# Optimization experiments

Hardware: AMD Instinct MI355X
Metric: run time of the kernel (lower is better)

The kernel has to match this reference:

```python
import jax, jax.numpy as jnp
import numpy as np

N, E = 50000, 800000
IN_DIM, OUT_DIM, H = 256, 128, 8
GEO_HID = 16  # RBF feature dim and geo_mlp hidden dim


def setup_inputs() -> dict:
    key = jax.random.key(0)
    ks = jax.random.split(key, 16)
    def lin(k, fan_out, fan_in):
        kw, kb = jax.random.split(k)
        lim = 1.0 / np.sqrt(fan_in)
        W = jax.random.uniform(kw, (fan_out, fan_in), jnp.float32, -lim, lim)
        b = jax.random.uniform(kb, (fan_out,), jnp.float32, -lim, lim)
        return W, b
    Wq, bq = lin(ks[0], OUT_DIM, IN_DIM)
    Wk, bk = lin(ks[1], OUT_DIM, IN_DIM)
    Wv, bv = lin(ks[2], OUT_DIM, IN_DIM)
    Wo, bo = lin(ks[3], OUT_DIM, OUT_DIM)
    Wg1, bg1 = lin(ks[4], GEO_HID, GEO_HID)
    Wg2, bg2 = lin(ks[5], H, GEO_HID)
    x = jax.random.normal(ks[6], (N, IN_DIM), jnp.float32)
    edge_index = jax.random.randint(ks[7], (2, E), 0, N, jnp.int64)
    edge_dist = jax.random.uniform(ks[8], (E,), jnp.float32) * 6.0
    return {"x": x, "edge_index": edge_index, "edge_dist": edge_dist,
            "Wq": Wq, "bq": bq, "Wk": Wk, "bk": bk, "Wv": Wv, "bv": bv,
            "Wo": Wo, "bo": bo, "Wg1": Wg1, "bg1": bg1, "Wg2": Wg2, "bg2": bg2}


def reference(x, edge_index, edge_dist, Wq, bq, Wk, bk, Wv, bv, Wo, bo, Wg1, bg1, Wg2, bg2):
    n = x.shape[0]
    num_heads = Wg2.shape[0]
    head_dim = Wq.shape[0] // num_heads
    scale = 1.0 / (head_dim ** 0.5)

    q = (x @ Wq.T + bq).reshape(n, num_heads, head_dim)
    k = (x @ Wk.T + bk).reshape(n, num_heads, head_dim)
    v = (x @ Wv.T + bv).reshape(n, num_heads, head_dim)

    # RBF expansion: 16 centers in [0, 6], gamma = 1.0
    centers = jnp.linspace(0.0, 6.0, GEO_HID)
    rbf = jnp.exp(-(edge_dist[:, None] - centers) ** 2)          # [E, 16]
    geo_bias = jax.nn.relu(rbf @ Wg1.T + bg1) @ Wg2.T + bg2      # [E, H]

    row, col = edge_index[0], edge_index[1]
    attn = (q[row] * k[col]).sum(-1) * scale + geo_bias          # [E, H]

    # segment softmax over incoming edges per destination node (row)
    m = jax.ops.segment_max(attn, row, num_segments=n)           # [N, H]
    e = jnp.exp(attn - m[row])
    s = jax.ops.segment_sum(e, row, num_segments=n)              # [N, H]
    a = e / (s[row] + 1e-12)                                     # [E, H]

    out = jax.ops.segment_sum(v[col] * a[:, :, None], row, num_segments=n)
    out = out.reshape(n, num_heads * head_dim)
    return out @ Wo.T + bo
```

## Files before the change

kernel.cpp:

```cpp
#include <hip/hip_runtime.h>
#include <math.h>

#define IN_DIM 256
#define OUT_DIM 128
#define NH 8
#define HD 16
#define GH 16
#define TBL 1024
#define LOG2E 1.44269504f
#define RCAP 64
#define BINSH 6
#define BCAP 1408

typedef __attribute__((ext_vector_type(8))) short short8;
typedef __attribute__((ext_vector_type(4))) float floatx4;

__device__ __forceinline__ unsigned short f2bf(float f) {
    union { float f; unsigned u; } v; v.f = f;
    unsigned r = v.u + 0x7fffu + ((v.u >> 16) & 1u);
    return (unsigned short)(r >> 16);
}
__device__ __forceinline__ float bf2f(unsigned short h) {
    union { unsigned u; float f; } v; v.u = ((unsigned)h) << 16;
    return v.f;
}
__device__ __forceinline__ void split1(float f, unsigned short& h, unsigned short& l) {
    h = f2bf(f);
    l = f2bf(f - bf2f(h));
}
__device__ __forceinline__ float bflo(unsigned u) { return __uint_as_float(u << 16); }
__device__ __forceinline__ float bfhi(unsigned u) { return __uint_as_float(u & 0xffff0000u); }

__global__ __launch_bounds__(256) void prep_all_kernel(
    const float* __restrict__ Wq, const float* __restrict__ Wk,
    const float* __restrict__ Wv, const float* __restrict__ Wo,
    unsigned short* __restrict__ wh, unsigned short* __restrict__ wl,
    unsigned short* __restrict__ wo_h, unsigned short* __restrict__ wo_l,
    const float* __restrict__ Wg1, const float* __restrict__ bg1,
    const float* __restrict__ Wg2, const float* __restrict__ bg2,
    float* __restrict__ tbl, int* __restrict__ gbin,
    int nbins, int nwm, int nwo, int ngeo) {
    int bx = blockIdx.x;
    int t = threadIdx.x;

    if (bx < 3 * nwm) {
        int m = bx / nwm;
        int i = (bx - m * nwm) * 256 + t;
        if (i >= (OUT_DIM * IN_DIM) / 4) return;
        const float* W = (m == 0) ? Wq : (m == 1) ? Wk : Wv;
        float4 f = ((const float4*)W)[i];
        ushort4 h, l;
        split1(f.x, h.x, l.x); split1(f.y, h.y, l.y);
        split1(f.z, h.z, l.z); split1(f.w, h.w, l.w);
        size_t base = (size_t)m * (OUT_DIM * IN_DIM) / 4;
        ((ushort4*)wh)[base + i] = h;
        ((ushort4*)wl)[base + i] = l;
        return;
    }
    bx -= 3 * nwm;
    if (bx < nwo) {
        int i = bx * 256 + t;
        if (i >= (OUT_DIM * OUT_DIM) / 4) return;
        float4 f = ((const float4*)Wo)[i];
        ushort4 h, l;
        split1(f.x, h.x, l.x); split1(f.y, h.y, l.y);
        split1(f.z, h.z, l.z); split1(f.w, h.w, l.w);
        ((ushort4*)wo_h)[i] = h;
        ((ushort4*)wo_l)[i] = l;
        return;
    }
    bx -= nwo;
    if (bx < ngeo) {
        int i = bx * 256 + t;
        if (i >= TBL) return;
        float d = (float)i * (6.0f / (float)(TBL - 1));
        float rbf[GH];
#pragma unroll
        for (int j = 0; j < GH; ++j) {
            float c = 0.4f * (float)j;
            float tt = d - c;
            rbf[j] = __expf(-tt * tt);
        }
        float hid[GH];
#pragma unroll
        for (int j = 0; j < GH; ++j) {
            float acc = bg1[j];
#pragma unroll
            for (int kk = 0; kk < GH; ++kk) acc += rbf[kk] * Wg1[j * GH + kk];
            hid[j] = fmaxf(acc, 0.0f);
        }
#pragma unroll
        for (int h = 0; h < NH; ++h) {
            float acc = bg2[h];
#pragma unroll
            for (int j = 0; j < GH; ++j) acc += hid[j] * Wg2[h * GH + j];
            tbl[i * NH + h] = acc * LOG2E;
        }
        return;
    }
    for (int i = t; i < nbins; i += 256) gbin[i] = 0;
}

__global__ __launch_bounds__(512, 4) void qkv_kernel(
    const float* __restrict__ x,
    const unsigned short* __restrict__ wh, const unsigned short* __restrict__ wl,
    const float* __restrict__ bq, const float* __restrict__ bk, const float* __restrict__ bv,
    float* __restrict__ q, unsigned short* __restrict__ kb, unsigned short* __restrict__ vb,
    const int* __restrict__ ei, const float* __restrict__ edist,
    int* __restrict__ gbin, int2* __restrict__ binbuf,
    int Nn, int E_, int nxb, int nb1, int nbins) {
    __shared__ unsigned short xh_s[128 * 40];
    __shared__ unsigned short xl_s[128 * 40];
    __shared__ unsigned short wh_s[128 * 40];
    __shared__ unsigned short wl_s[128 * 40];

    const int tid = threadIdx.x;
    int bx = blockIdx.x;

    if (bx < nb1) {
        int* hist_s = (int*)xh_s;
        const int e0 = bx * 4096;
        for (int b = tid; b < nbins; b += 512) hist_s[b] = 0;
        __syncthreads();
#pragma unroll
        for (int i = 0; i < 8; ++i) {
            int e = e0 + tid + i * 512;
            if (e < E_) atomicAdd(&hist_s[ei[e] >> BINSH], 1);
        }
        __syncthreads();
        for (int b = tid; b < nbins; b += 512) {
            int h = hist_s[b];
            int base = 0;
            if (h) base = atomicAdd(&gbin[b], h);
            hist_s[b] = base;
        }
        __syncthreads();
#pragma unroll
        for (int i = 0; i < 8; ++i) {
            int e = e0 + tid + i * 512;
            if (e < E_) {
                int row = ei[e];
                int bin = row >> BINSH;
                int r = atomicAdd(&hist_s[bin], 1);
                float u = edist[e] * ((float)(TBL - 1) / 6.0f);
                u = fminf(fmaxf(u, 0.0f), (float)(TBL - 1));
                if (r < BCAP)
                    binbuf[(size_t)bin * BCAP + r] =
                        make_int2((ei[E_ + e] & 0x1FFFF) | ((row & 63) << 17), __float_as_int(u));
            }
        }
        return;
    }
    bx -= nb1;

    const int wsel = bx / nxb;
    const int n0 = (bx - wsel * nxb) * 128;
    const unsigned short* W_h = wh + (size_t)wsel * (OUT_DIM * IN_DIM);
    const unsigned short* W_l = wl + (size_t)wsel * (OUT_DIM * IN_DIM);
    const float* bias = (wsel == 0) ? bq : (wsel == 1) ? bk : bv;
    const bool vpath = (wsel == 2);

    const int w = tid >> 6;
    const int lane = tid & 63;
    const int ml = lane & 15;
    const int quad = lane >> 4;
    const int rg = w & 3;
    const int cg = w >> 2;

    const int rows_valid = min(128, Nn - n0);

    floatx4 acc[2][4];
#pragma unroll
    for (int rr = 0; rr < 2; ++rr)
#pragma unroll
        for (int ct = 0; ct < 4; ++ct) acc[rr][ct] = (floatx4){0.f, 0.f, 0.f, 0.f};

    const int r = tid >> 2, c = tid & 3;
    const bool rvld = (r < rows_valid);
    const float* xrow = x + (size_t)(n0 + r) * IN_DIM + c * 8;
    const unsigned short* wrow_h = W_h + (size_t)r * IN_DIM + c * 8;
    const unsigned short* wrow_l = W_l + (size_t)r * IN_DIM + c * 8;

    float4 xa = {0.f, 0.f, 0.f, 0.f}, xb = {0.f, 0.f, 0.f, 0.f};
    short8 wreg_h, wreg_l;
    if (rvld) { xa = ((const float4*)xrow)[0]; xb = ((const float4*)xrow)[1]; }
    wreg_h = *(const short8*)(wrow_h);
    if (vpath) wreg_l = *(const short8*)(wrow_l);

    for (int kci = 0; kci < 8; ++kci) {
        {
            float xf[8] = {xa.x, xa.y, xa.z, xa.w, xb.x, xb.y, xb.z, xb.w};
            if (!vpath) {
                unsigned short hv[8];
#pragma unroll
                for (int j = 0; j < 8; ++j) hv[j] = f2bf(xf[j]);
                *(short8*)(xh_s + r * 40 + c * 8) = *(short8*)hv;
                *(short8*)(wh_s + r * 40 + c * 8) = wreg_h;
            } else {
                unsigned short hv[8], lv[8];
#pragma unroll
                for (int j = 0; j < 8; ++j) split1(xf[j], hv[j], lv[j]);
                *(short8*)(xh_s + r * 40 + c * 8) = *(short8*)hv;
                *(short8*)(xl_s + r * 40 + c * 8) = *(short8*)lv;
                *(short8*)(wh_s + r * 40 + c * 8) = wreg_h;
                *(short8*)(wl_s + r * 40 + c * 8) = wreg_l;
            }
        }
        __syncthreads();

        if (kci < 7) {
            const int koff = (kci + 1) * 32;
            if (rvld) {
                xa = ((const float4*)(xrow + koff))[0];
                xb = ((const float4*)(xrow + koff))[1];
            }
            wreg_h = *(const short8*)(wrow_h + koff);
            if (vpath) wreg_l = *(const short8*)(wrow_l + koff);
        }

        short8 ah0 = *(const short8*)(xh_s + (rg * 32 + ml) * 40 + quad * 8);
        short8 ah1 = *(const short8*)(xh_s + (rg * 32 + 16 + ml) * 40 + quad * 8);
        if (!vpath) {
#pragma unroll
            for (int ct = 0; ct < 4; ++ct) {
                short8 bh = *(const short8*)(wh_s + (cg * 64 + ct * 16 + ml) * 40 + quad * 8);
                acc[0][ct] = __builtin_amdgcn_mfma_f32_16x16x32_bf16(ah0, bh, acc[0][ct], 0, 0, 0);
                acc[1][ct] = __builtin_amdgcn_mfma_f32_16x16x32_bf16(ah1, bh, acc[1][ct], 0, 0, 0);
            }
        } else {
            short8 al0 = *(const short8*)(xl_s + (rg * 32 + ml) * 40 + quad * 8);
            short8 al1 = *(const short8*)(xl_s + (rg * 32 + 16 + ml) * 40 + quad * 8);
#pragma unroll
            for (int ct = 0; ct < 4; ++ct) {
                short8 bh = *(const short8*)(wh_s + (cg * 64 + ct * 16 + ml) * 40 + quad * 8);
                short8 bl = *(const short8*)(wl_s + (cg * 64 + ct * 16 + ml) * 40 + quad * 8);
                acc[0][ct] = __builtin_amdgcn_mfma_f32_16x16x32_bf16(ah0, bh, acc[0][ct], 0, 0, 0);
                acc[0][ct] = __builtin_amdgcn_mfma_f32_16x16x32_bf16(al0, bh, acc[0][ct], 0, 0, 0);
                acc[0][ct] = __builtin_amdgcn_mfma_f32_16x16x32_bf16(ah0, bl, acc[0][ct], 0, 0, 0);
                acc[1][ct] = __builtin_amdgcn_mfma_f32_16x16x32_bf16(ah1, bh, acc[1][ct], 0, 0, 0);
                acc[1][ct] = __builtin_amdgcn_mfma_f32_16x16x32_bf16(al1, bh, acc[1][ct], 0, 0, 0);
                acc[1][ct] = __builtin_amdgcn_mfma_f32_16x16x32_bf16(ah1, bl, acc[1][ct], 0, 0, 0);
            }
        }
        __syncthreads();
    }

    if (wsel == 0) {
#pragma unroll
        for (int rr = 0; rr < 2; ++rr)
#pragma unroll
            for (int ct = 0; ct < 4; ++ct) {
                int col = cg * 64 + ct * 16 + ml;
                float bj = bias[col];
#pragma unroll
                for (int rr2 = 0; rr2 < 4; ++rr2) {
                    int grow = n0 + rg * 32 + rr * 16 + quad * 4 + rr2;
                    if (grow < Nn) q[(size_t)grow * 128 + col] = acc[rr][ct][rr2] + bj;
                }
            }
    } else {
        unsigned short* ob = (wsel == 1) ? kb : vb;
#pragma unroll
        for (int rr = 0; rr < 2; ++rr)
#pragma unroll
            for (int ct = 0; ct < 4; ++ct) {
                int col = cg * 64 + ct * 16 + ml;
                float bj = bias[col];
#pragma unroll
                for (int rr2 = 0; rr2 < 4; ++rr2) {
                    int grow = n0 + rg * 32 + rr * 16 + quad * 4 + rr2;
                    if (grow < Nn) ob[(size_t)grow * 128 + col] = f2bf(acc[rr][ct][rr2] + bj);
                }
            }
    }
}

__global__ __launch_bounds__(256) void bin2bucket_kernel(
    const int2* __restrict__ binbuf, const int* __restrict__ gbin,
    int2* __restrict__ bucket, int2* __restrict__ meta, int Nn) {
    __shared__ int rcnt[64];
    __shared__ int pref[64];
    __shared__ int2 ebuf[BCAP];
    const int bin = blockIdx.x;
    const int t = threadIdx.x;
    if (t < 64) rcnt[t] = 0;
    __syncthreads();
    int nb = gbin[bin];
    if (nb > BCAP) nb = BCAP;
    const int row0 = bin << BINSH;

    int px[6], py[6], rk[6];
#pragma unroll
    for (int j = 0; j < 6; ++j) {
        int i = t + j * 256;
        rk[j] = -1;
        if (i < nb) {
            int2 p = binbuf[(size_t)bin * BCAP + i];
            int rowrel = (p.x >> 17) & 63;
            int r = atomicAdd(&rcnt[rowrel], 1);
            if (r < RCAP) { px[j] = p.x & 0x1FFFF; py[j] = p.y; rk[j] = r | (rowrel << 16); }
        }
    }
    __syncthreads();
    int myclamp = 0;
    if (t < 64) { myclamp = min(rcnt[t], RCAP); pref[t] = myclamp; }
    __syncthreads();
    for (int off = 1; off < 64; off <<= 1) {
        int v = 0;
        if (t < 64 && t >= off) v = pref[t - off];
        __syncthreads();
        if (t < 64) pref[t] += v;
        __syncthreads();
    }
#pragma unroll
    for (int j = 0; j < 6; ++j) {
        if (rk[j] >= 0) {
            int rowrel = rk[j] >> 16;
            int r = rk[j] & 0xFFFF;
            int pos = pref[rowrel] - min(rcnt[rowrel], RCAP) + r;
            ebuf[pos] = make_int2(px[j], py[j]);
        }
    }
    __syncthreads();
    int total = pref[63];
    const int obase = bin * BCAP;
    for (int i = t; i < total; i += 256) bucket[obase + i] = ebuf[i];
    if (t < 64 && row0 + t < Nn)
        meta[row0 + t] = make_int2(obase + pref[t] - myclamp, myclamp);
}

__global__ __launch_bounds__(256) void fused_node_kernel(
    const float* __restrict__ q, const unsigned short* __restrict__ kb,
    const unsigned short* __restrict__ vb, const int2* __restrict__ bucket,
    const float* __restrict__ tbl, const int2* __restrict__ meta,
    float* __restrict__ o, int Nn) {
    const int lane = threadIdx.x & 63;
    const int g = lane >> 3;
    const int h = lane & 7;
    const int n = blockIdx.x * 4 + (threadIdx.x >> 6);
    if (n >= Nn) return;

    const int2 m = meta[n];
    const int start = m.x;
    const int c = m.y;
    const int end = start + c;

    float qf[16];
    {
        const float4* qp = (const float4*)(q + (size_t)n * 128 + h * 16);
#pragma unroll
        for (int j = 0; j < 4; ++j) {
            float4 t = qp[j];
            qf[j * 4 + 0] = t.x; qf[j * 4 + 1] = t.y;
            qf[j * 4 + 2] = t.z; qf[j * 4 + 3] = t.w;
        }
    }

    float l = 0.0f;
    float acc[16];
#pragma unroll
    for (int j = 0; j < 16; ++j) acc[j] = 0.0f;

    auto edge_math = [&](const uint4& k0, const uint4& k1, const uint4& v0, const uint4& v1,
                         float u, bool valid) {
        unsigned kk[8] = {k0.x, k0.y, k0.z, k0.w, k1.x, k1.y, k1.z, k1.w};
        float d = 0.0f;
#pragma unroll
        for (int j = 0; j < 8; ++j) {
            d = fmaf(bflo(kk[j]), qf[2 * j], d);
            d = fmaf(bfhi(kk[j]), qf[2 * j + 1], d);
        }
        int i0 = min((int)u, TBL - 2);
        float fr = u - (float)i0;
        float t0 = tbl[i0 * NH + h];
        float t1 = tbl[i0 * NH + NH + h];
        float logit2 = fmaf(d, 0.25f * LOG2E, fmaf(fr, t1 - t0, t0));
        logit2 = fminf(logit2, 80.0f);
        if (!valid) logit2 = -1e30f;
        float p = __builtin_amdgcn_exp2f(logit2);
        l += p;
        unsigned vv[8] = {v0.x, v0.y, v0.z, v0.w, v1.x, v1.y, v1.z, v1.w};
#pragma unroll
        for (int j = 0; j < 8; ++j) {
            acc[2 * j]     = fmaf(p, bflo(vv[j]), acc[2 * j]);
            acc[2 * j + 1] = fmaf(p, bfhi(vv[j]), acc[2 * j + 1]);
        }
    };

    if (c > 0) {
        int2 npA = bucket[min(start + g, end - 1)];
        const bool vAv = (start + g < end);
        const bool doB = (end > start + 8);
        int2 npB = npA;
        bool vBv = false;
        if (doB) {
            npB = bucket[min(start + 8 + g, end - 1)];
            vBv = (start + 8 + g < end);
        }
        const uint4* kpA = (const uint4*)(kb + (size_t)npA.x * 128 + h * 16);
        const uint4* vpA = (const uint4*)(vb + (size_t)npA.x * 128 + h * 16);
        uint4 kA0 = kpA[0], kA1 = kpA[1], vA0 = vpA[0], vA1 = vpA[1];
        uint4 kB0, kB1, vB0, vB1;
        if (doB) {
            const uint4* kpB = (const uint4*)(kb + (size_t)npB.x * 128 + h * 16);
            const uint4* vpB = (const uint4*)(vb + (size_t)npB.x * 128 + h * 16);
            kB0 = kpB[0]; kB1 = kpB[1]; vB0 = vpB[0]; vB1 = vpB[1];
        }
        edge_math(kA0, kA1, vA0, vA1, __int_as_float(npA.y), vAv);
        if (doB) edge_math(kB0, kB1, vB0, vB1, __int_as_float(npB.y), vBv);
        for (int base = start + 16; base < end; base += 8) {
            int2 np = bucket[min(base + g, end - 1)];
            bool valid = (base + g < end);
            const uint4* kp = (const uint4*)(kb + (size_t)np.x * 128 + h * 16);
            const uint4* vp = (const uint4*)(vb + (size_t)np.x * 128 + h * 16);
            uint4 k0 = kp[0], k1 = kp[1], v0 = vp[0], v1 = vp[1];
            edge_math(k0, k1, v0, v1, __int_as_float(np.y), valid);
        }
    }

#pragma unroll
    for (int off = 8; off < 64; off <<= 1) {
        l += __shfl_xor(l, off);
#pragma unroll
        for (int j = 0; j < 16; ++j) acc[j] += __shfl_xor(acc[j], off);
    }

    if (g == 0) {
        float inv = 1.0f / (l + 1e-12f);
        float4* op = (float4*)(o + (size_t)n * 128 + h * 16);
#pragma unroll
        for (int j = 0; j < 4; ++j) {
            float4 t;
            t.x = acc[j * 4 + 0] * inv; t.y = acc[j * 4 + 1] * inv;
            t.z = acc[j * 4 + 2] * inv; t.w = acc[j * 4 + 3] * inv;
            op[j] = t;
        }
    }
}

__global__ __launch_bounds__(512, 4) void out_gemm_mfma_kernel(
    const float* __restrict__ o,
    const unsigned short* __restrict__ wo_h, const unsigned short* __restrict__ wo_l,
    const float* __restrict__ bo, float* __restrict__ out, int Nn) {
    const int n0 = blockIdx.x * 128;

    __shared__ unsigned short xh_s[128 * 40];
    __shared__ unsigned short xl_s[128 * 40];
    __shared__ unsigned short wh_s[128 * 40];
    __shared__ unsigned short wl_s[128 * 40];

    const int tid = threadIdx.x;
    const int w = tid >> 6;
    const int lane = tid & 63;
    const int ml = lane & 15;
    const int quad = lane >> 4;
    const int rg = w & 3;
    const int cg = w >> 2;

    const int rows_valid = min(128, Nn - n0);

    floatx4 acc[2][4];
#pragma unroll
    for (int rr = 0; rr < 2; ++rr)
#pragma unroll
        for (int ct = 0; ct < 4; ++ct) acc[rr][ct] = (floatx4){0.f, 0.f, 0.f, 0.f};

    const int r = tid >> 2, c = tid & 3;
    const bool rvld = (r < rows_valid);
    const float* orow = o + (size_t)(n0 + r) * OUT_DIM + c * 8;
    const unsigned short* wrow_h = wo_h + (size_t)r * OUT_DIM + c * 8;
    const unsigned short* wrow_l = wo_l + (size_t)r * OUT_DIM + c * 8;

    float4 oa = {0.f, 0.f, 0.f, 0.f}, ob2 = {0.f, 0.f, 0.f, 0.f};
    short8 wreg_h, wreg_l;
    if (rvld) { oa = ((const float4*)orow)[0]; ob2 = ((const float4*)orow)[1]; }
    wreg_h = *(const short8*)(wrow_h);
    wreg_l = *(const short8*)(wrow_l);

    for (int kci = 0; kci < 4; ++kci) {
        {
            float xf[8] = {oa.x, oa.y, oa.z, oa.w, ob2.x, ob2.y, ob2.z, ob2.w};
            unsigned short hv[8], lv[8];
#pragma unroll
            for (int j = 0; j < 8; ++j) split1(xf[j], hv[j], lv[j]);
            *(short8*)(xh_s + r * 40 + c * 8) = *(short8*)hv;
            *(short8*)(xl_s + r * 40 + c * 8) = *(short8*)lv;
            *(short8*)(wh_s + r * 40 + c * 8) = wreg_h;
            *(short8*)(wl_s + r * 40 + c * 8) = wreg_l;
        }
        __syncthreads();

        if (kci < 3) {
            const int koff = (kci + 1) * 32;
            if (rvld) {
                oa  = ((const float4*)(orow + koff))[0];
                ob2 = ((const float4*)(orow + koff))[1];
            }
            wreg_h = *(const short8*)(wrow_h + koff);
            wreg_l = *(const short8*)(wrow_l + koff);
        }

        short8 ah0 = *(const short8*)(xh_s + (rg * 32 + ml) * 40 + quad * 8);
        short8 ah1 = *(const short8*)(xh_s + (rg * 32 + 16 + ml) * 40 + quad * 8);
        short8 al0 = *(const short8*)(xl_s + (rg * 32 + ml) * 40 + quad * 8);
        short8 al1 = *(const short8*)(xl_s + (rg * 32 + 16 + ml) * 40 + quad * 8);
#pragma unroll
        for (int ct = 0; ct < 4; ++ct) {
            short8 bh = *(const short8*)(wh_s + (cg * 64 + ct * 16 + ml) * 40 + quad * 8);
            short8 bl = *(const short8*)(wl_s + (cg * 64 + ct * 16 + ml) * 40 + quad * 8);
            acc[0][ct] = __builtin_amdgcn_mfma_f32_16x16x32_bf16(ah0, bh, acc[0][ct], 0, 0, 0);
            acc[0][ct] = __builtin_amdgcn_mfma_f32_16x16x32_bf16(al0, bh, acc[0][ct], 0, 0, 0);
            acc[0][ct] = __builtin_amdgcn_mfma_f32_16x16x32_bf16(ah0, bl, acc[0][ct], 0, 0, 0);
            acc[1][ct] = __builtin_amdgcn_mfma_f32_16x16x32_bf16(ah1, bh, acc[1][ct], 0, 0, 0);
            acc[1][ct] = __builtin_amdgcn_mfma_f32_16x16x32_bf16(al1, bh, acc[1][ct], 0, 0, 0);
            acc[1][ct] = __builtin_amdgcn_mfma_f32_16x16x32_bf16(ah1, bl, acc[1][ct], 0, 0, 0);
        }
        __syncthreads();
    }

#pragma unroll
    for (int rr = 0; rr < 2; ++rr)
#pragma unroll
        for (int ct = 0; ct < 4; ++ct) {
            int col = cg * 64 + ct * 16 + ml;
            float bj = bo[col];
#pragma unroll
            for (int rr2 = 0; rr2 < 4; ++rr2) {
                int grow = n0 + rg * 32 + rr * 16 + quad * 4 + rr2;
                if (grow < Nn) out[(size_t)grow * 128 + col] = acc[rr][ct][rr2] + bj;
            }
        }
}

extern "C" void kernel_launch(void* const* d_in, const int* in_sizes, int n_in,
                              void* d_out, int out_size, void* d_ws, size_t ws_size,
                              hipStream_t stream) {
    const float* x   = (const float*)d_in[0];
    const int* ei    = (const int*)d_in[1];
    const float* edist = (const float*)d_in[2];
    const float* Wq = (const float*)d_in[3];  const float* bq = (const float*)d_in[4];
    const float* Wk = (const float*)d_in[5];  const float* bk = (const float*)d_in[6];
    const float* Wv = (const float*)d_in[7];  const float* bv = (const float*)d_in[8];
    const float* Wo = (const float*)d_in[9];  const float* bo = (const float*)d_in[10];
    const float* Wg1 = (const float*)d_in[11]; const float* bg1 = (const float*)d_in[12];
    const float* Wg2 = (const float*)d_in[13]; const float* bg2 = (const float*)d_in[14];
    const int Nn = in_sizes[0] / IN_DIM;
    const int Ee = in_sizes[2];
    float* out = (float*)d_out;

    char* ws = (char*)d_ws;
    size_t off = 0;
    auto alloc = [&](size_t bytes) -> char* {
        char* p = ws + off;
        off += (bytes + 255) & ~(size_t)255;
        return p;
    };
    float* q  = (float*)alloc((size_t)Nn * 128 * 4);
    unsigned short* kbuf = (unsigned short*)alloc((size_t)Nn * 128 * 2);
    unsigned short* vbuf = (unsigned short*)alloc((size_t)Nn * 128 * 2);
    float* o = (float*)alloc((size_t)Nn * 128 * 4);
    float* geot = (float*)alloc((size_t)TBL * 8 * 4);
    int2* meta = (int2*)alloc((size_t)Nn * 8);
    int nbins = (Nn + 63) >> BINSH;
    int* gbin = (int*)alloc((size_t)nbins * 4);
    unsigned short* wh_all = (unsigned short*)alloc((size_t)3 * OUT_DIM * IN_DIM * 2);
    unsigned short* wl_all = (unsigned short*)alloc((size_t)3 * OUT_DIM * IN_DIM * 2);
    unsigned short* wo_h = (unsigned short*)alloc((size_t)OUT_DIM * OUT_DIM * 2);
    unsigned short* wo_l = (unsigned short*)alloc((size_t)OUT_DIM * OUT_DIM * 2);
    int2* bucket = (int2*)alloc((size_t)nbins * BCAP * 8);

    int2* binbuf = (int2*)o;

    int nwm = ((OUT_DIM * IN_DIM / 4) + 255) / 256;
    int nwo = ((OUT_DIM * OUT_DIM / 4) + 255) / 256;
    int ngeo = (TBL + 255) / 256;
    int gprep = 3 * nwm + nwo + ngeo + 1;
    prep_all_kernel<<<gprep, 256, 0, stream>>>(
        Wq, Wk, Wv, Wo, wh_all, wl_all, wo_h, wo_l,
        Wg1, bg1, Wg2, bg2, geot, gbin, nbins, nwm, nwo, ngeo);

    int nxb = (Nn + 127) / 128;
    int nb1 = (Ee + 4095) / 4096;
    qkv_kernel<<<nb1 + 3 * nxb, 512, 0, stream>>>(
        x, wh_all, wl_all, bq, bk, bv, q, kbuf, vbuf,
        ei, edist, gbin, binbuf, Nn, Ee, nxb, nb1, nbins);

    bin2bucket_kernel<<<nbins, 256, 0, stream>>>(binbuf, gbin, bucket, meta, Nn);

    fused_node_kernel<<<(Nn + 3) / 4, 256, 0, stream>>>(q, kbuf, vbuf, bucket, geot, meta, o, Nn);

    out_gemm_mfma_kernel<<<(Nn + 127) / 128, 512, 0, stream>>>(o, wo_h, wo_l, bo, out, Nn);
}
```

Baseline: 252.5 us.

## Process two nodes per wave in attention kernel and shrink output GEMM tiles

The fused node kernel now assigns two destination nodes to each wavefront and interleaves their edge loops, so gathers for both nodes are in flight together. This is meant to hide gather latency and cut per-wave launch overhead, at the cost of doubled accumulator registers and possible imbalance when the two nodes have different degrees. The output GEMM moves from 128-row, 512-thread blocks to 64-row, 256-thread blocks, with each wave covering all 128 columns. This gives more blocks but loads the weight tile more times in total.

```diff
diff --git a/kernel.cpp b/kernel.cpp
--- a/kernel.cpp
+++ b/kernel.cpp
@@ -337,31 +337,42 @@
     const int lane = threadIdx.x & 63;
     const int g = lane >> 3;
     const int h = lane & 7;
-    const int n = blockIdx.x * 4 + (threadIdx.x >> 6);
-    if (n >= Nn) return;
-
-    const int2 m = meta[n];
-    const int start = m.x;
-    const int c = m.y;
-    const int end = start + c;
-
-    float qf[16];
+    const int wv = blockIdx.x * 4 + (threadIdx.x >> 6);
+    const int nA = wv * 2;
+    const int nB = nA + 1;
+    if (nA >= Nn) return;
+    const bool hasB = (nB < Nn);
+
+    const int2 mA = meta[nA];
+    const int2 mB = hasB ? meta[nB] : make_int2(0, 0);
+
+    float qfA[16], qfB[16];
     {
-        const float4* qp = (const float4*)(q + (size_t)n * 128 + h * 16);
+        const float4* qp = (const float4*)(q + (size_t)nA * 128 + h * 16);
 #pragma unroll
         for (int j = 0; j < 4; ++j) {
             float4 t = qp[j];
-            qf[j * 4 + 0] = t.x; qf[j * 4 + 1] = t.y;
-            qf[j * 4 + 2] = t.z; qf[j * 4 + 3] = t.w;
-        }
-    }
-
-    float l = 0.0f;
-    float acc[16];
-#pragma unroll
-    for (int j = 0; j < 16; ++j) acc[j] = 0.0f;
-
-    auto edge_math = [&](const uint4& k0, const uint4& k1, const uint4& v0, const uint4& v1,
+            qfA[j * 4 + 0] = t.x; qfA[j * 4 + 1] = t.y;
+            qfA[j * 4 + 2] = t.z; qfA[j * 4 + 3] = t.w;
+        }
+    }
+    if (hasB) {
+        const float4* qp = (const float4*)(q + (size_t)nB * 128 + h * 16);
+#pragma unroll
+        for (int j = 0; j < 4; ++j) {
+            float4 t = qp[j];
+            qfB[j * 4 + 0] = t.x; qfB[j * 4 + 1] = t.y;
+            qfB[j * 4 + 2] = t.z; qfB[j * 4 + 3] = t.w;
+        }
+    }
+
+    float lA = 0.0f, lB = 0.0f;
+    float accA[16], accB[16];
+#pragma unroll
+    for (int j = 0; j < 16; ++j) { accA[j] = 0.0f; accB[j] = 0.0f; }
+
+    auto edge_math = [&](const float* qf, float* acc, float& l,
+                         const uint4& k0, const uint4& k1, const uint4& v0, const uint4& v1,
                          float u, bool valid) {
         unsigned kk[8] = {k0.x, k0.y, k0.z, k0.w, k1.x, k1.y, k1.z, k1.w};
         float d = 0.0f;
@@ -387,65 +398,78 @@
         }
     };
 
-    if (c > 0) {
-        int2 npA = bucket[min(start + g, end - 1)];
-        const bool vAv = (start + g < end);
-        const bool doB = (end > start + 8);
-        int2 npB = npA;
-        bool vBv = false;
+    int baseA = mA.x;
+    const int endA = mA.x + mA.y;
+    int baseB = mB.x;
+    const int endB = mB.x + mB.y;
+
+    while (baseA < endA || baseB < endB) {
+        const bool doA = (baseA < endA);
+        const bool doB = (baseB < endB);
+        int2 npA, npB;
+        bool vA = false, vB = false;
+        if (doA) { npA = bucket[min(baseA + g, endA - 1)]; vA = (baseA + g < endA); }
+        if (doB) { npB = bucket[min(baseB + g, endB - 1)]; vB = (baseB + g < endB); }
+        uint4 kA0, kA1, vA0, vA1, kB0, kB1, vB0, vB1;
+        if (doA) {
+            const uint4* kp = (const uint4*)(kb + (size_t)npA.x * 128 + h * 16);
+            const uint4* vp = (const uint4*)(vb + (size_t)npA.x * 128 + h * 16);
+            kA0 = kp[0]; kA1 = kp[1]; vA0 = vp[0]; vA1 = vp[1];
+        }
         if (doB) {
-            npB = bucket[min(start + 8 + g, end - 1)];
-            vBv = (start + 8 + g < end);
-        }
-        const uint4* kpA = (const uint4*)(kb + (size_t)npA.x * 128 + h * 16);
-        const uint4* vpA = (const uint4*)(vb + (size_t)npA.x * 128 + h * 16);
-        uint4 kA0 = kpA[0], kA1 = kpA[1], vA0 = vpA[0], vA1 = vpA[1];
-        uint4 kB0, kB1, vB0, vB1;
-        if (doB) {
-            const uint4* kpB = (const uint4*)(kb + (size_t)npB.x * 128 + h * 16);
-            const uint4* vpB = (const uint4*)(vb + (size_t)npB.x * 128 + h * 16);
-            kB0 = kpB[0]; kB1 = kpB[1]; vB0 = vpB[0]; vB1 = vpB[1];
-        }
-        edge_math(kA0, kA1, vA0, vA1, __int_as_float(npA.y), vAv);
-        if (doB) edge_math(kB0, kB1, vB0, vB1, __int_as_float(npB.y), vBv);
-        for (int base = start + 16; base < end; base += 8) {
-            int2 np = bucket[min(base + g, end - 1)];
-            bool valid = (base + g < end);
-            const uint4* kp = (const uint4*)(kb + (size_t)np.x * 128 + h * 16);
-            const uint4* vp = (const uint4*)(vb + (size_t)np.x * 128 + h * 16);
-            uint4 k0 = kp[0], k1 = kp[1], v0 = vp[0], v1 = vp[1];
-            edge_math(k0, k1, v0, v1, __int_as_float(np.y), valid);
-        }
+            const uint4* kp = (const uint4*)(kb + (size_t)npB.x * 128 + h * 16);
+            const uint4* vp = (const uint4*)(vb + (size_t)npB.x * 128 + h * 16);
+            kB0 = kp[0]; kB1 = kp[1]; vB0 = vp[0]; vB1 = vp[1];
+        }
+        if (doA) { edge_math(qfA, accA, lA, kA0, kA1, vA0, vA1, __int_as_float(npA.y), vA); baseA += 8; }
+        if (doB) { edge_math(qfB, accB, lB, kB0, kB1, vB0, vB1, __int_as_float(npB.y), vB); baseB += 8; }
     }
 
 #pragma unroll
     for (int off = 8; off < 64; off <<= 1) {
-        l += __shfl_xor(l, off);
-#pragma unroll
-        for (int j = 0; j < 16; ++j) acc[j] += __shfl_xor(acc[j], off);
+        lA += __shfl_xor(lA, off);
+        lB += __shfl_xor(lB, off);
+#pragma unroll
+        for (int j = 0; j < 16; ++j) {
+            accA[j] += __shfl_xor(accA[j], off);
+            accB[j] += __shfl_xor(accB[j], off);
+        }
     }
 
     if (g == 0) {
-        float inv = 1.0f / (l + 1e-12f);
-        float4* op = (float4*)(o + (size_t)n * 128 + h * 16);
-#pragma unroll
-        for (int j = 0; j < 4; ++j) {
-            float4 t;
-            t.x = acc[j * 4 + 0] * inv; t.y = acc[j * 4 + 1] * inv;
-            t.z = acc[j * 4 + 2] * inv; t.w = acc[j * 4 + 3] * inv;
-            op[j] = t;
-        }
-    }
-}
-
-__global__ __launch_bounds__(512, 4) void out_gemm_mfma_kernel(
+        {
+            float inv = 1.0f / (lA + 1e-12f);
+            float4* op = (float4*)(o + (size_t)nA * 128 + h * 16);
+#pragma unroll
+            for (int j = 0; j < 4; ++j) {
+                float4 t;
+                t.x = accA[j * 4 + 0] * inv; t.y = accA[j * 4 + 1] * inv;
+                t.z = accA[j * 4 + 2] * inv; t.w = accA[j * 4 + 3] * inv;
+                op[j] = t;
+            }
+        }
+        if (hasB) {
+            float inv = 1.0f / (lB + 1e-12f);
+            float4* op = (float4*)(o + (size_t)nB * 128 + h * 16);
+#pragma unroll
+            for (int j = 0; j < 4; ++j) {
+                float4 t;
+                t.x = accB[j * 4 + 0] * inv; t.y = accB[j * 4 + 1] * inv;
+                t.z = accB[j * 4 + 2] * inv; t.w = accB[j * 4 + 3] * inv;
+                op[j] = t;
+            }
+        }
+    }
+}
+
+__global__ __launch_bounds__(256) void out_gemm_mfma_kernel(
     const float* __restrict__ o,
     const unsigned short* __restrict__ wo_h, const unsigned short* __restrict__ wo_l,
     const float* __restrict__ bo, float* __restrict__ out, int Nn) {
-    const int n0 = blockIdx.x * 128;
-
-    __shared__ unsigned short xh_s[128 * 40];
-    __shared__ unsigned short xl_s[128 * 40];
+    const int n0 = blockIdx.x * 64;
+
+    __shared__ unsigned short xh_s[64 * 40];
+    __shared__ unsigned short xl_s[64 * 40];
     __shared__ unsigned short wh_s[128 * 40];
     __shared__ unsigned short wl_s[128 * 40];
 
@@ -454,28 +478,28 @@
     const int lane = tid & 63;
     const int ml = lane & 15;
     const int quad = lane >> 4;
-    const int rg = w & 3;
-    const int cg = w >> 2;
-
-    const int rows_valid = min(128, Nn - n0);
-
-    floatx4 acc[2][4];
-#pragma unroll
-    for (int rr = 0; rr < 2; ++rr)
-#pragma unroll
-        for (int ct = 0; ct < 4; ++ct) acc[rr][ct] = (floatx4){0.f, 0.f, 0.f, 0.f};
+
+    const int rows_valid = min(64, Nn - n0);
+
+    floatx4 acc[8];
+#pragma unroll
+    for (int ct = 0; ct < 8; ++ct) acc[ct] = (floatx4){0.f, 0.f, 0.f, 0.f};
 
     const int r = tid >> 2, c = tid & 3;
     const bool rvld = (r < rows_valid);
     const float* orow = o + (size_t)(n0 + r) * OUT_DIM + c * 8;
-    const unsigned short* wrow_h = wo_h + (size_t)r * OUT_DIM + c * 8;
-    const unsigned short* wrow_l = wo_l + (size_t)r * OUT_DIM + c * 8;
+    const int rW0 = tid >> 2, cW0 = tid & 3;
+    const int rW1 = rW0 + 64, cW1 = cW0;
+    const unsigned short* w0h = wo_h + (size_t)rW0 * OUT_DIM + cW0 * 8;
+    const unsigned short* w0l = wo_l + (size_t)rW0 * OUT_DIM + cW0 * 8;
+    const unsigned short* w1h = wo_h + (size_t)rW1 * OUT_DIM + cW1 * 8;
+    const unsigned short* w1l = wo_l + (size_t)rW1 * OUT_DIM + cW1 * 8;
 
     float4 oa = {0.f, 0.f, 0.f, 0.f}, ob2 = {0.f, 0.f, 0.f, 0.f};
-    short8 wreg_h, wreg_l;
+    short8 wr0h, wr0l, wr1h, wr1l;
     if (rvld) { oa = ((const float4*)orow)[0]; ob2 = ((const float4*)orow)[1]; }
-    wreg_h = *(const short8*)(wrow_h);
-    wreg_l = *(const short8*)(wrow_l);
+    wr0h = *(const short8*)w0h; wr0l = *(const short8*)w0l;
+    wr1h = *(const short8*)w1h; wr1l = *(const short8*)w1l;
 
     for (int kci = 0; kci < 4; ++kci) {
         {
@@ -485,8 +509,10 @@
             for (int j = 0; j < 8; ++j) split1(xf[j], hv[j], lv[j]);
             *(short8*)(xh_s + r * 40 + c * 8) = *(short8*)hv;
             *(short8*)(xl_s + r * 40 + c * 8) = *(short8*)lv;
-            *(short8*)(wh_s + r * 40 + c * 8) = wreg_h;
-            *(short8*)(wl_s + r * 40 + c * 8) = wreg_l;
+            *(short8*)(wh_s + rW0 * 40 + cW0 * 8) = wr0h;
+            *(short8*)(wl_s + rW0 * 40 + cW0 * 8) = wr0l;
+            *(short8*)(wh_s + rW1 * 40 + cW1 * 8) = wr1h;
+            *(short8*)(wl_s + rW1 * 40 + cW1 * 8) = wr1l;
         }
         __syncthreads();
 
@@ -496,40 +522,32 @@
                 oa  = ((const float4*)(orow + koff))[0];
                 ob2 = ((const float4*)(orow + koff))[1];
             }
-            wreg_h = *(const short8*)(wrow_h + koff);
-            wreg_l = *(const short8*)(wrow_l + koff);
-        }
-
-        short8 ah0 = *(const short8*)(xh_s + (rg * 32 + ml) * 40 + quad * 8);
-        short8 ah1 = *(const short8*)(xh_s + (rg * 32 + 16 + ml) * 40 + quad * 8);
-        short8 al0 = *(const short8*)(xl_s + (rg * 32 + ml) * 40 + quad * 8);
-        short8 al1 = *(const short8*)(xl_s + (rg * 32 + 16 + ml) * 40 + quad * 8);
-#pragma unroll
-        for (int ct = 0; ct < 4; ++ct) {
-            short8 bh = *(const short8*)(wh_s + (cg * 64 + ct * 16 + ml) * 40 + quad * 8);
-            short8 bl = *(const short8*)(wl_s + (cg * 64 + ct * 16 + ml) * 40 + quad * 8);
-            acc[0][ct] = __builtin_amdgcn_mfma_f32_16x16x32_bf16(ah0, bh, acc[0][ct], 0, 0, 0);
-            acc[0][ct] = __builtin_amdgcn_mfma_f32_16x16x32_bf16(al0, bh, acc[0][ct], 0, 0, 0);
-            acc[0][ct] = __builtin_amdgcn_mfma_f32_16x16x32_bf16(ah0, bl, acc[0][ct], 0, 0, 0);
-            acc[1][ct] = __builtin_amdgcn_mfma_f32_16x16x32_bf16(ah1, bh, acc[1][ct], 0, 0, 0);
-            acc[1][ct] = __builtin_amdgcn_mfma_f32_16x16x32_bf16(al1, bh, acc[1][ct], 0, 0, 0);
-            acc[1][ct] = __builtin_amdgcn_mfma_f32_16x16x32_bf16(ah1, bl, acc[1][ct], 0, 0, 0);
-        }
-        __syncthreads();
-    }
-
-#pragma unroll
-    for (int rr = 0; rr < 2; ++rr)
-#pragma unroll
-        for (int ct = 0; ct < 4; ++ct) {
-            int col = cg * 64 + ct * 16 + ml;
-            float bj = bo[col];
-#pragma unroll
-            for (int rr2 = 0; rr2 < 4; ++rr2) {
-                int grow = n0 + rg * 32 + rr * 16 + quad * 4 + rr2;
-                if (grow < Nn) out[(size_t)grow * 128 + col] = acc[rr][ct][rr2] + bj;
-            }
-        }
+            wr0h = *(const short8*)(w0h + koff); wr0l = *(const short8*)(w0l + koff);
+            wr1h = *(const short8*)(w1h + koff); wr1l = *(const short8*)(w1l + koff);
+        }
+
+        short8 ah = *(const short8*)(xh_s + (w * 16 + ml) * 40 + quad * 8);
+        short8 al = *(const short8*)(xl_s + (w * 16 + ml) * 40 + quad * 8);
+#pragma unroll
+        for (int ct = 0; ct < 8; ++ct) {
+            short8 bh = *(const short8*)(wh_s + (ct * 16 + ml) * 40 + quad * 8);
+            short8 bl = *(const short8*)(wl_s + (ct * 16 + ml) * 40 + quad * 8);
+            acc[ct] = __builtin_amdgcn_mfma_f32_16x16x32_bf16(ah, bh, acc[ct], 0, 0, 0);
+            acc[ct] = __builtin_amdgcn_mfma_f32_16x16x32_bf16(al, bh, acc[ct], 0, 0, 0);
+            acc[ct] = __builtin_amdgcn_mfma_f32_16x16x32_bf16(ah, bl, acc[ct], 0, 0, 0);
+        }
+        __syncthreads();
+    }
+
+#pragma unroll
+    for (int ct = 0; ct < 8; ++ct) {
+        float bj = bo[ct * 16 + ml];
+#pragma unroll
+        for (int rr2 = 0; rr2 < 4; ++rr2) {
+            int grow = n0 + w * 16 + quad * 4 + rr2;
+            if (grow < Nn) out[(size_t)grow * 128 + ct * 16 + ml] = acc[ct][rr2] + bj;
+        }
+    }
 }
 
 extern "C" void kernel_launch(void* const* d_in, const int* in_sizes, int n_in,
@@ -587,7 +605,10 @@
 
     bin2bucket_kernel<<<nbins, 256, 0, stream>>>(binbuf, gbin, bucket, meta, Nn);
 
-    fused_node_kernel<<<(Nn + 3) / 4, 256, 0, stream>>>(q, kbuf, vbuf, bucket, geot, meta, o, Nn);
-
-    out_gemm_mfma_kernel<<<(Nn + 127) / 128, 512, 0, stream>>>(o, wo_h, wo_l, bo, out, Nn);
-}
+    {
+        int nwaves = (Nn + 1) / 2;
+        fused_node_kernel<<<(nwaves + 3) / 4, 256, 0, stream>>>(q, kbuf, vbuf, bucket, geot, meta, o, Nn);
+    }
+
+    out_gemm_mfma_kernel<<<(Nn + 63) / 64, 256, 0, stream>>>(o, wo_h, wo_l, bo, out, Nn);
+}
```

New measurement: 271.2 us. +7.4%, slower.

## Move V projection GEMM into bin-to-bucket kernel to overlap with scatter

Applied to the files above, without the earlier changes.

The V projection (split-bf16, three MFMAs per step) leaves the Q/K kernel and is fused into the bin-to-bucket kernel as extra blocks. Bucketing blocks, which are latency- and atomics-bound, now run beside compute-heavy V GEMM blocks. The Q/K kernel also drops its unused lo-part shared buffers, which lowers its LDS use and may raise occupancy. The risk is that the combined kernel needs the larger LDS footprint for every block, bucketing blocks included, and that the bucketing path now uses 512 threads.

```diff
diff --git a/kernel.cpp b/kernel.cpp
--- a/kernel.cpp
+++ b/kernel.cpp
@@ -101,18 +101,16 @@
     for (int i = t; i < nbins; i += 256) gbin[i] = 0;
 }
 
-__global__ __launch_bounds__(512, 4) void qkv_kernel(
+__global__ __launch_bounds__(512, 4) void qk_kernel(
     const float* __restrict__ x,
-    const unsigned short* __restrict__ wh, const unsigned short* __restrict__ wl,
-    const float* __restrict__ bq, const float* __restrict__ bk, const float* __restrict__ bv,
-    float* __restrict__ q, unsigned short* __restrict__ kb, unsigned short* __restrict__ vb,
+    const unsigned short* __restrict__ wh,
+    const float* __restrict__ bq, const float* __restrict__ bk,
+    float* __restrict__ q, unsigned short* __restrict__ kb,
     const int* __restrict__ ei, const float* __restrict__ edist,
     int* __restrict__ gbin, int2* __restrict__ binbuf,
     int Nn, int E_, int nxb, int nb1, int nbins) {
     __shared__ unsigned short xh_s[128 * 40];
-    __shared__ unsigned short xl_s[128 * 40];
     __shared__ unsigned short wh_s[128 * 40];
-    __shared__ unsigned short wl_s[128 * 40];
 
     const int tid = threadIdx.x;
     int bx = blockIdx.x;
@@ -156,9 +154,7 @@
     const int wsel = bx / nxb;
     const int n0 = (bx - wsel * nxb) * 128;
     const unsigned short* W_h = wh + (size_t)wsel * (OUT_DIM * IN_DIM);
-    const unsigned short* W_l = wl + (size_t)wsel * (OUT_DIM * IN_DIM);
-    const float* bias = (wsel == 0) ? bq : (wsel == 1) ? bk : bv;
-    const bool vpath = (wsel == 2);
+    const float* bias = (wsel == 0) ? bq : bk;
 
     const int w = tid >> 6;
     const int lane = tid & 63;
@@ -179,32 +175,20 @@
     const bool rvld = (r < rows_valid);
     const float* xrow = x + (size_t)(n0 + r) * IN_DIM + c * 8;
     const unsigned short* wrow_h = W_h + (size_t)r * IN_DIM + c * 8;
-    const unsigned short* wrow_l = W_l + (size_t)r * IN_DIM + c * 8;
 
     float4 xa = {0.f, 0.f, 0.f, 0.f}, xb = {0.f, 0.f, 0.f, 0.f};
-    short8 wreg_h, wreg_l;
+    short8 wreg_h;
     if (rvld) { xa = ((const float4*)xrow)[0]; xb = ((const float4*)xrow)[1]; }
     wreg_h = *(const short8*)(wrow_h);
-    if (vpath) wreg_l = *(const short8*)(wrow_l);
 
     for (int kci = 0; kci < 8; ++kci) {
         {
             float xf[8] = {xa.x, xa.y, xa.z, xa.w, xb.x, xb.y, xb.z, xb.w};
-            if (!vpath) {
-                unsigned short hv[8];
-#pragma unroll
-                for (int j = 0; j < 8; ++j) hv[j] = f2bf(xf[j]);
-                *(short8*)(xh_s + r * 40 + c * 8) = *(short8*)hv;
-                *(short8*)(wh_s + r * 40 + c * 8) = wreg_h;
-            } else {
-                unsigned short hv[8], lv[8];
-#pragma unroll
-                for (int j = 0; j < 8; ++j) split1(xf[j], hv[j], lv[j]);
-                *(short8*)(xh_s + r * 40 + c * 8) = *(short8*)hv;
-                *(short8*)(xl_s + r * 40 + c * 8) = *(short8*)lv;
-                *(short8*)(wh_s + r * 40 + c * 8) = wreg_h;
-                *(short8*)(wl_s + r * 40 + c * 8) = wreg_l;
-            }
+            unsigned short hv[8];
+#pragma unroll
+            for (int j = 0; j < 8; ++j) hv[j] = f2bf(xf[j]);
+            *(short8*)(xh_s + r * 40 + c * 8) = *(short8*)hv;
+            *(short8*)(wh_s + r * 40 + c * 8) = wreg_h;
         }
         __syncthreads();
 
@@ -215,32 +199,15 @@
                 xb = ((const float4*)(xrow + koff))[1];
             }
             wreg_h = *(const short8*)(wrow_h + koff);
-            if (vpath) wreg_l = *(const short8*)(wrow_l + koff);
         }
 
         short8 ah0 = *(const short8*)(xh_s + (rg * 32 + ml) * 40 + quad * 8);
         short8 ah1 = *(const short8*)(xh_s + (rg * 32 + 16 + ml) * 40 + quad * 8);
-        if (!vpath) {
-#pragma unroll
-            for (int ct = 0; ct < 4; ++ct) {
-                short8 bh = *(const short8*)(wh_s + (cg * 64 + ct * 16 + ml) * 40 + quad * 8);
-                acc[0][ct] = __builtin_amdgcn_mfma_f32_16x16x32_bf16(ah0, bh, acc[0][ct], 0, 0, 0);
-                acc[1][ct] = __builtin_amdgcn_mfma_f32_16x16x32_bf16(ah1, bh, acc[1][ct], 0, 0, 0);
-            }
-        } else {
-            short8 al0 = *(const short8*)(xl_s + (rg * 32 + ml) * 40 + quad * 8);
-            short8 al1 = *(const short8*)(xl_s + (rg * 32 + 16 + ml) * 40 + quad * 8);
-#pragma unroll
-            for (int ct = 0; ct < 4; ++ct) {
-                short8 bh = *(const short8*)(wh_s + (cg * 64 + ct * 16 + ml) * 40 + quad * 8);
-                short8 bl = *(const short8*)(wl_s + (cg * 64 + ct * 16 + ml) * 40 + quad * 8);
-                acc[0][ct] = __builtin_amdgcn_mfma_f32_16x16x32_bf16(ah0, bh, acc[0][ct], 0, 0, 0);
-                acc[0][ct] = __builtin_amdgcn_mfma_f32_16x16x32_bf16(al0, bh, acc[0][ct], 0, 0, 0);
-                acc[0][ct] = __builtin_amdgcn_mfma_f32_16x16x32_bf16(ah0, bl, acc[0][ct], 0, 0, 0);
-                acc[1][ct] = __builtin_amdgcn_mfma_f32_16x16x32_bf16(ah1, bh, acc[1][ct], 0, 0, 0);
-                acc[1][ct] = __builtin_amdgcn_mfma_f32_16x16x32_bf16(al1, bh, acc[1][ct], 0, 0, 0);
-                acc[1][ct] = __builtin_amdgcn_mfma_f32_16x16x32_bf16(ah1, bl, acc[1][ct], 0, 0, 0);
-            }
+#pragma unroll
+        for (int ct = 0; ct < 4; ++ct) {
+            short8 bh = *(const short8*)(wh_s + (cg * 64 + ct * 16 + ml) * 40 + quad * 8);
+            acc[0][ct] = __builtin_amdgcn_mfma_f32_16x16x32_bf16(ah0, bh, acc[0][ct], 0, 0, 0);
+            acc[1][ct] = __builtin_amdgcn_mfma_f32_16x16x32_bf16(ah1, bh, acc[1][ct], 0, 0, 0);
         }
         __syncthreads();
     }
@@ -259,7 +226,6 @@
                 }
             }
     } else {
-        unsigned short* ob = (wsel == 1) ? kb : vb;
 #pragma unroll
         for (int rr = 0; rr < 2; ++rr)
 #pragma unroll
@@ -269,64 +235,165 @@
 #pragma unroll
                 for (int rr2 = 0; rr2 < 4; ++rr2) {
                     int grow = n0 + rg * 32 + rr * 16 + quad * 4 + rr2;
-                    if (grow < Nn) ob[(size_t)grow * 128 + col] = f2bf(acc[rr][ct][rr2] + bj);
+                    if (grow < Nn) kb[(size_t)grow * 128 + col] = f2bf(acc[rr][ct][rr2] + bj);
                 }
             }
     }
 }
 
-__global__ __launch_bounds__(256) void bin2bucket_kernel(
+__global__ __launch_bounds__(512, 4) void v_b2b_kernel(
+    const float* __restrict__ x,
+    const unsigned short* __restrict__ wh, const unsigned short* __restrict__ wl,
+    const float* __restrict__ bv, unsigned short* __restrict__ vb,
     const int2* __restrict__ binbuf, const int* __restrict__ gbin,
-    int2* __restrict__ bucket, int2* __restrict__ meta, int Nn) {
-    __shared__ int rcnt[64];
-    __shared__ int pref[64];
-    __shared__ int2 ebuf[BCAP];
-    const int bin = blockIdx.x;
-    const int t = threadIdx.x;
-    if (t < 64) rcnt[t] = 0;
-    __syncthreads();
-    int nb = gbin[bin];
-    if (nb > BCAP) nb = BCAP;
-    const int row0 = bin << BINSH;
-
-    int px[6], py[6], rk[6];
-#pragma unroll
-    for (int j = 0; j < 6; ++j) {
-        int i = t + j * 256;
-        rk[j] = -1;
-        if (i < nb) {
-            int2 p = binbuf[(size_t)bin * BCAP + i];
-            int rowrel = (p.x >> 17) & 63;
-            int r = atomicAdd(&rcnt[rowrel], 1);
-            if (r < RCAP) { px[j] = p.x & 0x1FFFF; py[j] = p.y; rk[j] = r | (rowrel << 16); }
-        }
-    }
-    __syncthreads();
-    int myclamp = 0;
-    if (t < 64) { myclamp = min(rcnt[t], RCAP); pref[t] = myclamp; }
-    __syncthreads();
-    for (int off = 1; off < 64; off <<= 1) {
-        int v = 0;
-        if (t < 64 && t >= off) v = pref[t - off];
-        __syncthreads();
-        if (t < 64) pref[t] += v;
-        __syncthreads();
-    }
-#pragma unroll
-    for (int j = 0; j < 6; ++j) {
-        if (rk[j] >= 0) {
-            int rowrel = rk[j] >> 16;
-            int r = rk[j] & 0xFFFF;
-            int pos = pref[rowrel] - min(rcnt[rowrel], RCAP) + r;
-            ebuf[pos] = make_int2(px[j], py[j]);
-        }
-    }
-    __syncthreads();
-    int total = pref[63];
-    const int obase = bin * BCAP;
-    for (int i = t; i < total; i += 256) bucket[obase + i] = ebuf[i];
-    if (t < 64 && row0 + t < Nn)
-        meta[row0 + t] = make_int2(obase + pref[t] - myclamp, myclamp);
+    int2* __restrict__ bucket, int2* __restrict__ meta,
+    int Nn, int nxb, int nbins) {
+    __shared__ unsigned short lds_u[4 * 128 * 40];
+
+    const int tid = threadIdx.x;
+    int bx = blockIdx.x;
+
+    if (bx < nbins) {
+        int* rcnt = (int*)lds_u;
+        int* pref = rcnt + 64;
+        int2* ebuf = (int2*)(pref + 64);
+        const int bin = bx;
+        if (tid < 64) rcnt[tid] = 0;
+        __syncthreads();
+        int nb = gbin[bin];
+        if (nb > BCAP) nb = BCAP;
+        const int row0 = bin << BINSH;
+
+        int px[3], py[3], rk[3];
+#pragma unroll
+        for (int j = 0; j < 3; ++j) {
+            int i = tid + j * 512;
+            rk[j] = -1;
+            if (i < nb) {
+                int2 p = binbuf[(size_t)bin * BCAP + i];
+                int rowrel = (p.x >> 17) & 63;
+                int r = atomicAdd(&rcnt[rowrel], 1);
+                if (r < RCAP) { px[j] = p.x & 0x1FFFF; py[j] = p.y; rk[j] = r | (rowrel << 16); }
+            }
+        }
+        __syncthreads();
+        int myclamp = 0;
+        if (tid < 64) { myclamp = min(rcnt[tid], RCAP); pref[tid] = myclamp; }
+        __syncthreads();
+        for (int off = 1; off < 64; off <<= 1) {
+            int v = 0;
+            if (tid < 64 && tid >= off) v = pref[tid - off];
+            __syncthreads();
+            if (tid < 64) pref[tid] += v;
+            __syncthreads();
+        }
+#pragma unroll
+        for (int j = 0; j < 3; ++j) {
+            if (rk[j] >= 0) {
+                int rowrel = rk[j] >> 16;
+                int r = rk[j] & 0xFFFF;
+                ebuf[pref[rowrel] - min(rcnt[rowrel], RCAP) + r] = make_int2(px[j], py[j]);
+            }
+        }
+        __syncthreads();
+        int total = pref[63];
+        const int obase = bin * BCAP;
+        for (int i = tid; i < total; i += 512) bucket[obase + i] = ebuf[i];
+        if (tid < 64 && row0 + tid < Nn)
+            meta[row0 + tid] = make_int2(obase + pref[tid] - myclamp, myclamp);
+        return;
+    }
+    bx -= nbins;
+
+    unsigned short* xh_s = lds_u;
+    unsigned short* xl_s = lds_u + 128 * 40;
+    unsigned short* wh_s = lds_u + 2 * 128 * 40;
+    unsigned short* wl_s = lds_u + 3 * 128 * 40;
+
+    const int n0 = bx * 128;
+    const unsigned short* W_h = wh + (size_t)2 * (OUT_DIM * IN_DIM);
+    const unsigned short* W_l = wl + (size_t)2 * (OUT_DIM * IN_DIM);
+
+    const int w = tid >> 6;
+    const int lane = tid & 63;
+    const int ml = lane & 15;
+    const int quad = lane >> 4;
+    const int rg = w & 3;
+    const int cg = w >> 2;
+
+    const int rows_valid = min(128, Nn - n0);
+
+    floatx4 acc[2][4];
+#pragma unroll
+    for (int rr = 0; rr < 2; ++rr)
+#pragma unroll
+        for (int ct = 0; ct < 4; ++ct) acc[rr][ct] = (floatx4){0.f, 0.f, 0.f, 0.f};
+
+    const int r = tid >> 2, c = tid & 3;
+    const bool rvld = (r < rows_valid);
+    const float* xrow = x + (size_t)(n0 + r) * IN_DIM + c * 8;
+    const unsigned short* wrow_h = W_h + (size_t)r * IN_DIM + c * 8;
+    const unsigned short* wrow_l = W_l + (size_t)r * IN_DIM + c * 8;
+
+    float4 xa = {0.f, 0.f, 0.f, 0.f}, xb = {0.f, 0.f, 0.f, 0.f};
+    short8 wreg_h, wreg_l;
+    if (rvld) { xa = ((const float4*)xrow)[0]; xb = ((const float4*)xrow)[1]; }
+    wreg_h = *(const short8*)(wrow_h);
+    wreg_l = *(const short8*)(wrow_l);
+
+    for (int kci = 0; kci < 8; ++kci) {
+        {
+            float xf[8] = {xa.x, xa.y, xa.z, xa.w, xb.x, xb.y, xb.z, xb.w};
+            unsigned short hv[8], lv[8];
+#pragma unroll
+            for (int j = 0; j < 8; ++j) split1(xf[j], hv[j], lv[j]);
+            *(short8*)(xh_s + r * 40 + c * 8) = *(short8*)hv;
+            *(short8*)(xl_s + r * 40 + c * 8) = *(short8*)lv;
+            *(short8*)(wh_s + r * 40 + c * 8) = wreg_h;
+            *(short8*)(wl_s + r * 40 + c * 8) = wreg_l;
+        }
+        __syncthreads();
+
+        if (kci < 7) {
+            const int koff = (kci + 1) * 32;
+            if (rvld) {
+                xa = ((const float4*)(xrow + koff))[0];
+                xb = ((const float4*)(xrow + koff))[1];
+            }
+            wreg_h = *(const short8*)(wrow_h + koff);
+            wreg_l = *(const short8*)(wrow_l + koff);
+        }
+
+        short8 ah0 = *(const short8*)(xh_s + (rg * 32 + ml) * 40 + quad * 8);
+        short8 ah1 = *(const short8*)(xh_s + (rg * 32 + 16 + ml) * 40 + quad * 8);
+        short8 al0 = *(const short8*)(xl_s + (rg * 32 + ml) * 40 + quad * 8);
+        short8 al1 = *(const short8*)(xl_s + (rg * 32 + 16 + ml) * 40 + quad * 8);
+#pragma unroll
+        for (int ct = 0; ct < 4; ++ct) {
+            short8 bh = *(const short8*)(wh_s + (cg * 64 + ct * 16 + ml) * 40 + quad * 8);
+            short8 bl = *(const short8*)(wl_s + (cg * 64 + ct * 16 + ml) * 40 + quad * 8);
+            acc[0][ct] = __builtin_amdgcn_mfma_f32_16x16x32_bf16(ah0, bh, acc[0][ct], 0, 0, 0);
+            acc[0][ct] = __builtin_amdgcn_mfma_f32_16x16x32_bf16(al0, bh, acc[0][ct], 0, 0, 0);
+            acc[0][ct] = __builtin_amdgcn_mfma_f32_16x16x32_bf16(ah0, bl, acc[0][ct], 0, 0, 0);
+            acc[1][ct] = __builtin_amdgcn_mfma_f32_16x16x32_bf16(ah1, bh, acc[1][ct], 0, 0, 0);
+            acc[1][ct] = __builtin_amdgcn_mfma_f32_16x16x32_bf16(al1, bh, acc[1][ct], 0, 0, 0);
+            acc[1][ct] = __builtin_amdgcn_mfma_f32_16x16x32_bf16(ah1, bl, acc[1][ct], 0, 0, 0);
+        }
+        __syncthreads();
+    }
+
+#pragma unroll
+    for (int rr = 0; rr < 2; ++rr)
+#pragma unroll
+        for (int ct = 0; ct < 4; ++ct) {
+            int col = cg * 64 + ct * 16 + ml;
+            float bj = bv[col];
+#pragma unroll
+            for (int rr2 = 0; rr2 < 4; ++rr2) {
+                int grow = n0 + rg * 32 + rr * 16 + quad * 4 + rr2;
+                if (grow < Nn) vb[(size_t)grow * 128 + col] = f2bf(acc[rr][ct][rr2] + bj);
+            }
+        }
 }
 
 __global__ __launch_bounds__(256) void fused_node_kernel(
@@ -581,11 +648,12 @@
 
     int nxb = (Nn + 127) / 128;
     int nb1 = (Ee + 4095) / 4096;
-    qkv_kernel<<<nb1 + 3 * nxb, 512, 0, stream>>>(
-        x, wh_all, wl_all, bq, bk, bv, q, kbuf, vbuf,
+    qk_kernel<<<nb1 + 2 * nxb, 512, 0, stream>>>(
+        x, wh_all, bq, bk, q, kbuf,
         ei, edist, gbin, binbuf, Nn, Ee, nxb, nb1, nbins);
 
-    bin2bucket_kernel<<<nbins, 256, 0, stream>>>(binbuf, gbin, bucket, meta, Nn);
+    v_b2b_kernel<<<nbins + nxb, 512, 0, stream>>>(
+        x, wh_all, wl_all, bv, vbuf, binbuf, gbin, bucket, meta, Nn, nxb, nbins);
 
     fused_node_kernel<<<(Nn + 3) / 4, 256, 0, stream>>>(q, kbuf, vbuf, bucket, geot, meta, o, Nn);
 
```

New measurement: 254.1 us. Within noise of the previous version (+0.6%).
